# Performance work log

Hardware: AMD Instinct MI355X
Metric: run time of the kernel (lower is better)

## Reference

```python
import jax, jax.numpy as jnp
import numpy as np
from jax import lax

BN_EPS = 1e-5


def ternarize(w):
    """Per-output-channel ternary quantization (Li & Liu TWN style).
    delta_i = 0.7 * mean(|w_i|); alpha_i = mean of |w| over entries with |w| > delta_i;
    output = alpha_i * (+1 where w > delta_i, -1 where w < -delta_i, else 0).
    """
    aw = jnp.abs(w)
    axes = tuple(range(1, w.ndim))
    delta = 0.7 * jnp.mean(aw, axis=axes)            # [O]
    d = delta.reshape((-1,) + (1,) * (w.ndim - 1))   # broadcastable
    mask = aw > d
    alpha = jnp.sum(aw * mask, axis=axes) / jnp.sum(mask, axis=axes)
    tern = jnp.where(w > d, 1.0, 0.0) - jnp.where(w < -d, 1.0, 0.0)
    return tern * alpha.reshape(d.shape)


def batchnorm2d(x, gamma, beta):
    # training-mode batchnorm: batch statistics over (N, H, W), biased variance
    mean = jnp.mean(x, axis=(0, 2, 3), keepdims=True)
    var = jnp.mean((x - mean) ** 2, axis=(0, 2, 3), keepdims=True)
    xhat = (x - mean) * lax.rsqrt(var + BN_EPS)
    return xhat * gamma[None, :, None, None] + beta[None, :, None, None]


def conv2d(x, w, b):
    out = lax.conv_general_dilated(x, w, window_strides=(1, 1), padding='VALID',
                                   dimension_numbers=('NCHW', 'OIHW', 'NCHW'))
    return out + b[None, :, None, None]


def maxpool2(x):
    return lax.reduce_window(x, -jnp.inf, lax.max, (1, 1, 2, 2), (1, 1, 2, 2), 'VALID')


def setup_inputs() -> dict:
    key = jax.random.key(0)
    ks = jax.random.split(key, 10)
    B = 4096
    return {
        'x': jax.random.normal(ks[0], (B, 1, 28, 28), jnp.float32),
        'w_conv1': jax.random.normal(ks[1], (32, 1, 5, 5), jnp.float32) * 0.2,
        'b_conv1': jax.random.normal(ks[2], (32,), jnp.float32) * 0.1,
        'gamma1': jnp.ones((32,), jnp.float32),
        'beta1': jnp.zeros((32,), jnp.float32),
        'w_conv2': jax.random.normal(ks[3], (64, 32, 5, 5), jnp.float32) * 0.05,
        'b_conv2': jax.random.normal(ks[4], (64,), jnp.float32) * 0.1,
        'gamma2': jnp.ones((64,), jnp.float32),
        'beta2': jnp.zeros((64,), jnp.float32),
        'w_fc1': jax.random.normal(ks[5], (512, 1024), jnp.float32) * 0.03,
        'b_fc1': jax.random.normal(ks[6], (512,), jnp.float32) * 0.1,
        'w_fc2': jax.random.normal(ks[7], (10, 512), jnp.float32) * 0.05,
        'b_fc2': jax.random.normal(ks[8], (10,), jnp.float32) * 0.1,
    }


def reference(x, w_conv1, b_conv1, gamma1, beta1, w_conv2, b_conv2, gamma2, beta2,
              w_fc1, b_fc1, w_fc2, b_fc2):
    h = conv2d(x, ternarize(w_conv1), b_conv1)          # [B,32,24,24]
    h = jax.nn.relu(maxpool2(batchnorm2d(h, gamma1, beta1)))  # [B,32,12,12]
    h = conv2d(h, ternarize(w_conv2), b_conv2)          # [B,64,8,8]
    h = jax.nn.relu(maxpool2(batchnorm2d(h, gamma2, beta2)))  # [B,64,4,4]
    h = h.reshape(-1, 1024)
    h = jax.nn.relu(h @ ternarize(w_fc1).T + b_fc1)     # [B,512]
    return h @ ternarize(w_fc2).T + b_fc2               # [B,10]
```

## Files before the change

### kernel.cpp

```cpp
#include <hip/hip_runtime.h>

#define TID ((int)threadIdx.x)
typedef unsigned short ushort_t;
typedef short short8 __attribute__((ext_vector_type(8)));
typedef float f32x4 __attribute__((ext_vector_type(4)));

__device__ __forceinline__ float bf2f(ushort_t u) {
    return __uint_as_float(((unsigned int)u) << 16);
}
__device__ __forceinline__ ushort_t f2bf(float f) {
    unsigned int x = __float_as_uint(f);
    return (ushort_t)((x + 0x7FFFu + ((x >> 16) & 1u)) >> 16);
}
__device__ __forceinline__ float ld1(const void* p, int i, bool f32) {
    return f32 ? ((const float*)p)[i] : bf2f(((const ushort_t*)p)[i]);
}
__device__ __forceinline__ bool probe_f32(const void* g1) {
    return ((const ushort_t*)g1)[0] == 0x0000u;
}

__global__ __launch_bounds__(256) void tern_all_kernel(
    const void* __restrict__ w1, const void* __restrict__ w2,
    const void* __restrict__ wf1, const void* __restrict__ wf2,
    float* __restrict__ o1, float* __restrict__ o2,
    float* __restrict__ of1, float* __restrict__ of2,
    float* __restrict__ stats_z, const void* __restrict__ g1probe)
{
    const bool f32 = probe_f32(g1probe);
    const int blk = blockIdx.x;
    if (blk < 48) stats_z[blk * 256 + TID] = 0.f;

    const void* w; float* out; int K, sk, so, o;
    if (blk < 32)       { w = w1;  out = o1;  K = 25;   sk = 1;  so = 25;   o = blk; }
    else if (blk < 96)  { w = w2;  out = o2;  K = 800;  sk = 64; so = 1;    o = blk - 32; }
    else if (blk < 608) { w = wf1; out = of1; K = 1024; sk = 1;  so = 1024; o = blk - 96; }
    else                { w = wf2; out = of2; K = 512;  sk = 1;  so = 512;  o = blk - 608; }

    const size_t base = (size_t)o * K;
    __shared__ float red[256];
    __shared__ float red2[256];

    float s = 0.f;
    for (int k = TID; k < K; k += 256) s += fabsf(ld1(w, base + k, f32));
    red[TID] = s; __syncthreads();
    for (int st = 128; st > 0; st >>= 1) {
        if (TID < st) red[TID] += red[TID + st];
        __syncthreads();
    }
    const float delta = 0.7f * red[0] / (float)K;
    __syncthreads();

    float ms = 0.f, cnt = 0.f;
    for (int k = TID; k < K; k += 256) {
        float aw = fabsf(ld1(w, base + k, f32));
        if (aw > delta) { ms += aw; cnt += 1.f; }
    }
    red[TID] = ms; red2[TID] = cnt; __syncthreads();
    for (int st = 128; st > 0; st >>= 1) {
        if (TID < st) { red[TID] += red[TID + st]; red2[TID] += red2[TID + st]; }
        __syncthreads();
    }
    const float denom = red2[0];
    const float alpha = (denom > 0.f) ? (red[0] / denom) : 0.f;

    for (int k = TID; k < K; k += 256) {
        float v = ld1(w, base + k, f32);
        float t = (v > delta) ? alpha : ((v < -delta) ? -alpha : 0.f);
        out[(size_t)k * sk + (size_t)o * so] = t;
    }
}

__global__ __launch_bounds__(256) void pack_all_kernel(
    const float* __restrict__ w1t, const float* __restrict__ w2t,
    const float* __restrict__ wf1t, const float* __restrict__ wf2t,
    short8* __restrict__ wpack1, short8* __restrict__ wpack2,
    short8* __restrict__ wf1pack, short8* __restrict__ wf2pack)
{
    const int blk = blockIdx.x;
    if (blk == 0) {
        if (TID < 128) {
            const int nt = TID >> 6, lane = TID & 63;
            const int n = nt * 16 + (lane & 15);
            const int qd = lane >> 4;
            short8 frag;
#pragma unroll
            for (int j = 0; j < 8; ++j) {
                int k = qd * 8 + j, ky = k / 6, kx = k - ky * 6;
                frag[j] = (k < 30 && kx < 5)
                          ? (short)f2bf(w1t[n * 25 + ky * 5 + kx]) : (short)0;
            }
            wpack1[nt * 64 + lane] = frag;
        }
    } else if (blk < 26) {
        const int pos = blk - 1;
        const int nt = TID >> 6, lane = TID & 63;
        const int oc = nt * 16 + (lane & 15);
        short8 frag;
#pragma unroll
        for (int j = 0; j < 8; ++j) {
            int ic = ((lane >> 4) << 3) + j;
            frag[j] = (short)f2bf(w2t[(ic * 25 + pos) * 64 + oc]);
        }
        wpack2[(pos * 4 + nt) * 64 + lane] = frag;
    } else if (blk < 282) {
        const int g = (blk - 26) * 256 + TID;
        const int lane = g & 63;
        const int ntg = (g >> 6) & 31;
        const int kk = g >> 11;
        const int n = ntg * 16 + (lane & 15);
        const int k0 = kk * 32 + ((lane >> 4) << 3);
        short8 frag;
#pragma unroll
        for (int j = 0; j < 8; ++j)
            frag[j] = (short)f2bf(wf1t[(size_t)n * 1024 + k0 + j]);
        wf1pack[g] = frag;
    } else {
        const int lane = TID & 63;
        const int n = lane & 15, qd = lane >> 4;
        for (int kk = TID >> 6; kk < 16; kk += 4) {
            short8 frag;
#pragma unroll
            for (int j = 0; j < 8; ++j)
                frag[j] = (n < 10)
                          ? (short)f2bf(wf2t[n * 512 + kk * 32 + qd * 8 + j])
                          : (short)0;
            wf2pack[kk * 64 + lane] = frag;
        }
    }
}

__device__ __forceinline__ void conv1_koff(int qd, int* koff) {
#pragma unroll
    for (int j = 0; j < 8; ++j) {
        int k = qd * 8 + j, ky = k / 6, kx = k - ky * 6;
        koff[j] = (k < 30 && kx < 5) ? (ky * 28 + kx) : -1;
    }
}

__global__ __launch_bounds__(256) void conv1_stats_kernel(
    const void* __restrict__ x, const short8* __restrict__ wpack1,
    const void* __restrict__ gamma1, float* __restrict__ stats,
    ushort_t* __restrict__ pooled1)
{
    const bool f32 = probe_f32(gamma1);
    __shared__ ushort_t xs[2][784];
    __shared__ float reds[4][64];
    const int b0 = blockIdx.x * 2;
    for (int c = TID; c < 392; c += 256) {
        const int img = (c >= 196) ? 1 : 0;
        const int cc = c - img * 196;
        if (f32) {
            float4 v4 = ((const float4*)x)[(size_t)(b0 + img) * 196 + cc];
            ushort4 u;
            u.x = f2bf(v4.x); u.y = f2bf(v4.y); u.z = f2bf(v4.z); u.w = f2bf(v4.w);
            *(ushort4*)&xs[img][cc * 4] = u;
        } else {
            *(ushort4*)&xs[img][cc * 4] =
                ((const ushort4*)x)[(size_t)(b0 + img) * 196 + cc];
        }
    }
    __syncthreads();

    const int lane = TID & 63, wv = TID >> 6;
    const int img = wv >> 1, wvi = wv & 1;
    const int qd = lane >> 4, ln15 = lane & 15;
    int koff[8];
    conv1_koff(qd, koff);
    const short8 bw0 = wpack1[lane];
    const short8 bw1 = wpack1[64 + lane];
    const bool pos0 = ld1(gamma1, ln15, f32) >= 0.f;
    const bool pos1 = ld1(gamma1, 16 + ln15, f32) >= 0.f;

    float s0 = 0.f, q0 = 0.f, s1 = 0.f, q1 = 0.f;
    const int cellA0 = (ln15 >> 2);
    const int m3 = ln15 & 3;
    const size_t pb = (size_t)(b0 + img) * 144;
    const ushort_t* xsi = xs[img];
    for (int t = wvi * 18; t < wvi * 18 + 18; ++t) {
        const int cellA = t * 4 + cellA0;
        const int pbase = ((cellA / 12) * 2 + (m3 >> 1)) * 28
                        + (cellA % 12) * 2 + (m3 & 1);
        short8 a;
#pragma unroll
        for (int j = 0; j < 8; ++j)
            a[j] = (koff[j] >= 0) ? (short)xsi[pbase + koff[j]] : (short)0;
        f32x4 c0 = {0.f, 0.f, 0.f, 0.f}, c1 = {0.f, 0.f, 0.f, 0.f};
        c0 = __builtin_amdgcn_mfma_f32_16x16x32_bf16(a, bw0, c0, 0, 0, 0);
        c1 = __builtin_amdgcn_mfma_f32_16x16x32_bf16(a, bw1, c1, 0, 0, 0);
#pragma unroll
        for (int r = 0; r < 4; ++r) {
            s0 += c0[r]; q0 += c0[r] * c0[r];
            s1 += c1[r]; q1 += c1[r] * c1[r];
        }
        float mx0 = fmaxf(fmaxf(c0[0], c0[1]), fmaxf(c0[2], c0[3]));
        float mn0 = fminf(fminf(c0[0], c0[1]), fminf(c0[2], c0[3]));
        float mx1 = fmaxf(fmaxf(c1[0], c1[1]), fmaxf(c1[2], c1[3]));
        float mn1 = fminf(fminf(c1[0], c1[1]), fminf(c1[2], c1[3]));
        const int cell = t * 4 + qd;
        pooled1[(pb + cell) * 32 + ln15]      = f2bf(pos0 ? mx0 : mn0);
        pooled1[(pb + cell) * 32 + 16 + ln15] = f2bf(pos1 ? mx1 : mn1);
    }
    s0 += __shfl_xor(s0, 16); q0 += __shfl_xor(q0, 16);
    s1 += __shfl_xor(s1, 16); q1 += __shfl_xor(q1, 16);
    s0 += __shfl_xor(s0, 32); q0 += __shfl_xor(q0, 32);
    s1 += __shfl_xor(s1, 32); q1 += __shfl_xor(q1, 32);
    if (lane < 16) {
        reds[wv][ln15]      = s0;
        reds[wv][32 + ln15] = q0;
        reds[wv][16 + ln15] = s1;
        reds[wv][48 + ln15] = q1;
    }
    __syncthreads();
    if (TID < 64) {
        float v = reds[0][TID] + reds[1][TID] + reds[2][TID] + reds[3][TID];
        atomicAdd(&stats[(blockIdx.x & 63) * 64 + TID], v);
    }
}

__global__ void bnfin_kernel(const float* __restrict__ stats, int C, int slots,
                             float invN,
                             const void* __restrict__ gamma,
                             const void* __restrict__ beta,
                             const void* __restrict__ bias,
                             float* __restrict__ sc, float* __restrict__ sh,
                             const void* __restrict__ g1probe)
{
    const bool f32 = probe_f32(g1probe);
    const int c = TID;
    if (c < C) {
        float s = 0.f, q = 0.f;
        for (int sl = 0; sl < slots; ++sl) {
            s += stats[sl * 2 * C + c];
            q += stats[sl * 2 * C + C + c];
        }
        float mraw = s * invN;
        float var  = q * invN - mraw * mraw;
        float mean = mraw + (bias ? ld1(bias, c, f32) : 0.f);
        float rstd = rsqrtf(fmaxf(var, 0.f) + 1e-5f);
        float g = ld1(gamma, c, f32) * rstd;
        sc[c] = g;
        sh[c] = ld1(beta, c, f32) - mean * g;
    }
}

__global__ __launch_bounds__(256) void conv12_kernel(
    const ushort_t* __restrict__ pooled1,
    const void* __restrict__ b1, const float* __restrict__ sc1,
    const float* __restrict__ sh1, const short8* __restrict__ wpack2,
    const void* __restrict__ b2, const void* __restrict__ gamma2,
    ushort_t* __restrict__ pooled2, float* __restrict__ stats2,
    const void* __restrict__ g1probe)
{
    const bool f32 = probe_f32(g1probe);
    __shared__ ushort_t p1b[144 * 40];
    __shared__ float r2[4][64];
    __shared__ float as1[32], hs1[32];
    const int b = blockIdx.x;
    if (TID < 32) {
        float a = sc1[TID];
        as1[TID] = a;
        hs1[TID] = fmaf(ld1(b1, TID, f32), a, sh1[TID]);
    }
    __syncthreads();

    {
        const uint* pm = (const uint*)(pooled1 + (size_t)b * 4608);
        const int ch2 = (TID * 2) & 31;
        const float aA = as1[ch2],     hA = hs1[ch2];
        const float aB = as1[ch2 + 1], hB = hs1[ch2 + 1];
#pragma unroll
        for (int i = 0; i < 9; ++i) {
            const int idx = i * 256 + TID;
            const uint u = pm[idx];
            const int cell = idx >> 4;
            float v0 = bf2f((ushort_t)(u & 0xFFFFu));
            float v1 = bf2f((ushort_t)(u >> 16));
            uint o0 = f2bf(fmaxf(fmaf(aA, v0, hA), 0.f));
            uint o1 = f2bf(fmaxf(fmaf(aB, v1, hB), 0.f));
            *(uint*)&p1b[cell * 40 + ch2] = o0 | (o1 << 16);
        }
    }
    __syncthreads();

    const int lane = TID & 63, wv = TID >> 6;
    const int qd = lane >> 4, ln15 = lane & 15;
    const int mh = wv >> 1, nh = wv & 1;
    const int px0 = (mh * 2 + 0) * 16 + ln15;
    const int px1 = (mh * 2 + 1) * 16 + ln15;
    const int base0 = (px0 >> 3) * 12 + (px0 & 7);
    const int base1 = (px1 >> 3) * 12 + (px1 & 7);

    f32x4 acc[2][2] = {};
#pragma unroll
    for (int pos = 0; pos < 25; ++pos) {
        const int koff2 = (pos / 5) * 12 + (pos % 5);
        short8 a0 = *(const short8*)&p1b[(base0 + koff2) * 40 + qd * 8];
        short8 a1 = *(const short8*)&p1b[(base1 + koff2) * 40 + qd * 8];
        short8 bb0 = wpack2[(pos * 4 + nh * 2 + 0) * 64 + lane];
        short8 bb1 = wpack2[(pos * 4 + nh * 2 + 1) * 64 + lane];
        acc[0][0] = __builtin_amdgcn_mfma_f32_16x16x32_bf16(a0, bb0, acc[0][0], 0, 0, 0);
        acc[0][1] = __builtin_amdgcn_mfma_f32_16x16x32_bf16(a0, bb1, acc[0][1], 0, 0, 0);
        acc[1][0] = __builtin_amdgcn_mfma_f32_16x16x32_bf16(a1, bb0, acc[1][0], 0, 0, 0);
        acc[1][1] = __builtin_amdgcn_mfma_f32_16x16x32_bf16(a1, bb1, acc[1][1], 0, 0, 0);
    }

    const size_t p2base = (size_t)b * 1024;
#pragma unroll
    for (int jn = 0; jn < 2; ++jn) {
        const int oc = (nh * 2 + jn) * 16 + ln15;
        const float bias = ld1(b2, oc, f32);
        const bool gpos = ld1(gamma2, oc, f32) >= 0.f;
        float s0 = 0.f, q0 = 0.f;
#pragma unroll
        for (int i = 0; i < 2; ++i) {
            float v0 = acc[i][jn][0] + bias;
            float v1 = acc[i][jn][1] + bias;
            float v2 = acc[i][jn][2] + bias;
            float v3 = acc[i][jn][3] + bias;
            s0 += v0 + v1 + v2 + v3;
            q0 += v0*v0 + v1*v1 + v2*v2 + v3*v3;
            float mx01 = fmaxf(v0, v1), mn01 = fminf(v0, v1);
            float mx23 = fmaxf(v2, v3), mn23 = fminf(v2, v3);
            mx01 = fmaxf(mx01, __shfl_xor(mx01, 32));
            mn01 = fminf(mn01, __shfl_xor(mn01, 32));
            mx23 = fmaxf(mx23, __shfl_xor(mx23, 32));
            mn23 = fminf(mn23, __shfl_xor(mn23, 32));
            if (qd < 2) {
                ushort2 st;
                st.x = f2bf(gpos ? mx01 : mn01);
                st.y = f2bf(gpos ? mx23 : mn23);
                const int ti = mh * 2 + i;
                *(ushort2*)&pooled2[p2base + (size_t)oc * 16 + ti * 4 + 2 * qd] = st;
            }
        }
        s0 += __shfl_down(s0, 32); q0 += __shfl_down(q0, 32);
        s0 += __shfl_down(s0, 16); q0 += __shfl_down(q0, 16);
        if (lane < 16) {
            r2[wv][jn * 32 + lane]      = s0;
            r2[wv][jn * 32 + 16 + lane] = q0;
        }
    }
    __syncthreads();
    if (TID < 128) {
        const int idx = TID & 63, nh2 = TID >> 6;
        float v = r2[nh2][idx] + r2[nh2 + 2][idx];
        const int jn = idx >> 5, isq = (idx >> 4) & 1, chx = idx & 15;
        const int oc = nh2 * 32 + jn * 16 + chx;
        atomicAdd(&stats2[(blockIdx.x & 63) * 128 + isq * 64 + oc], v);
    }
}

__global__ __launch_bounds__(256) void fc1_kernel(
    const ushort_t* __restrict__ pooled2, const short8* __restrict__ wf1pack,
    const float* __restrict__ sc2, const float* __restrict__ sh2,
    const void* __restrict__ bias, ushort_t* __restrict__ out,
    const void* __restrict__ g1probe)
{
    const bool f32 = probe_f32(g1probe);
    __shared__ ushort_t As[64 * 136];
    __shared__ float a2s[64], h2s[64];
    const int m0 = blockIdx.y * 64;
    const int n0x4 = blockIdx.x * 4;
    const int lane = TID & 63;
    const int wv   = TID >> 6;
    const int mh = wv >> 1, nh = wv & 1;
    const int qd = lane >> 4, ln15 = lane & 15;
    if (TID < 64) { a2s[TID] = sc2[TID]; h2s[TID] = sh2[TID]; }

    f32x4 acc[2][2] = {};
    for (int stage = 0; stage < 8; ++stage) {
        __syncthreads();
#pragma unroll
        for (int i = 0; i < 4; ++i) {
            const int idx = i * 256 + TID;
            const int row = idx >> 4, ch = idx & 15;
            const int k = stage * 128 + ch * 8;
            const int oc = k >> 4;
            const float a2 = a2s[oc], h2 = h2s[oc];
            uint4 u = *(const uint4*)&pooled2[(size_t)(m0 + row) * 1024 + k];
            uint4 o;
            uint* up = &u.x; uint* op = &o.x;
#pragma unroll
            for (int q = 0; q < 4; ++q) {
                float lo = bf2f((ushort_t)(up[q] & 0xFFFFu));
                float hi = bf2f((ushort_t)(up[q] >> 16));
                uint olo = f2bf(fmaxf(fmaf(a2, lo, h2), 0.f));
                uint ohi = f2bf(fmaxf(fmaf(a2, hi, h2), 0.f));
                op[q] = olo | (ohi << 16);
            }
            *(uint4*)&As[row * 136 + ch * 8] = o;
        }
        __syncthreads();
#pragma unroll
        for (int ks = 0; ks < 4; ++ks) {
            const int kk = stage * 4 + ks;
            const int col = ks * 32 + qd * 8;
            short8 a0 = *(const short8*)&As[(mh * 32 + ln15) * 136 + col];
            short8 a1 = *(const short8*)&As[(mh * 32 + 16 + ln15) * 136 + col];
            short8 bb0 = wf1pack[(kk * 32 + n0x4 + nh * 2 + 0) * 64 + lane];
            short8 bb1 = wf1pack[(kk * 32 + n0x4 + nh * 2 + 1) * 64 + lane];
            acc[0][0] = __builtin_amdgcn_mfma_f32_16x16x32_bf16(a0, bb0, acc[0][0], 0, 0, 0);
            acc[0][1] = __builtin_amdgcn_mfma_f32_16x16x32_bf16(a0, bb1, acc[0][1], 0, 0, 0);
            acc[1][0] = __builtin_amdgcn_mfma_f32_16x16x32_bf16(a1, bb0, acc[1][0], 0, 0, 0);
            acc[1][1] = __builtin_amdgcn_mfma_f32_16x16x32_bf16(a1, bb1, acc[1][1], 0, 0, 0);
        }
    }

#pragma unroll
    for (int jn = 0; jn < 2; ++jn) {
        const int n = n0x4 * 16 + (nh * 2 + jn) * 16 + ln15;
        const float bv = ld1(bias, n, f32);
#pragma unroll
        for (int i = 0; i < 2; ++i) {
            const int mb = m0 + (mh * 2 + i) * 16 + qd * 4;
#pragma unroll
            for (int r = 0; r < 4; ++r) {
                float v = fmaxf(acc[i][jn][r] + bv, 0.f);
                out[(size_t)(mb + r) * 512 + n] = f2bf(v);
            }
        }
    }
}

__global__ __launch_bounds__(256) void fc2_kernel(
    const ushort_t* __restrict__ h, const short8* __restrict__ wf2pack,
    const void* __restrict__ bias, void* __restrict__ out,
    const void* __restrict__ g1probe)
{
    const bool f32 = probe_f32(g1probe);
    const int lane = TID & 63, wv = TID >> 6;
    const int qd = lane >> 4, ln15 = lane & 15;
    const int m0 = (blockIdx.x * 4 + wv) * 16;

    f32x4 acc = {0.f, 0.f, 0.f, 0.f};
#pragma unroll
    for (int kk = 0; kk < 16; ++kk) {
        short8 a = *(const short8*)&h[(size_t)(m0 + ln15) * 512 + kk * 32 + qd * 8];
        acc = __builtin_amdgcn_mfma_f32_16x16x32_bf16(a, wf2pack[kk * 64 + lane],
                                                      acc, 0, 0, 0);
    }
    if (ln15 < 10) {
        const float bv = ld1(bias, ln15, f32);
#pragma unroll
        for (int r = 0; r < 4; ++r) {
            const size_t oi = (size_t)(m0 + qd * 4 + r) * 10 + ln15;
            float v = acc[r] + bv;
            if (f32) ((float*)out)[oi] = v;
            else ((ushort_t*)out)[oi] = f2bf(v);
        }
    }
}

extern "C" void kernel_launch(void* const* d_in, const int* in_sizes, int n_in,
                              void* d_out, int out_size, void* d_ws, size_t ws_size,
                              hipStream_t stream)
{
    const void* x       = d_in[0];
    const void* w_conv1 = d_in[1];
    const void* b_conv1 = d_in[2];
    const void* gamma1  = d_in[3];
    const void* beta1   = d_in[4];
    const void* w_conv2 = d_in[5];
    const void* b_conv2 = d_in[6];
    const void* gamma2  = d_in[7];
    const void* beta2   = d_in[8];
    const void* w_fc1   = d_in[9];
    const void* b_fc1   = d_in[10];
    const void* w_fc2   = d_in[11];
    const void* b_fc2   = d_in[12];

    char* wsb = (char*)d_ws;
    size_t off = 0;
    auto alloc = [&](size_t bytes) -> void* {
        void* p = wsb + off;
        off += (bytes + 255) & ~(size_t)255;
        return p;
    };

    float*  stats   = (float*)alloc(49152);
    float*  stats2  = stats + 4096;
    float*  sc1     = (float*)alloc(128);
    float*  sh1     = (float*)alloc(128);
    float*  sc2     = (float*)alloc(256);
    float*  sh2     = (float*)alloc(256);
    float*  w1t     = (float*)alloc(32 * 25 * 4);
    float*  w2t     = (float*)alloc(800 * 64 * 4);
    float*  wf1t    = (float*)alloc((size_t)512 * 1024 * 4);
    float*  wf2t    = (float*)alloc(10 * 512 * 4);
    short8* wpack1  = (short8*)alloc(2 * 64 * 16);
    short8* wpack2  = (short8*)alloc(25 * 4 * 64 * 16);
    short8* wf1pack = (short8*)alloc((size_t)32 * 32 * 64 * 16);
    short8* wf2pack = (short8*)alloc(16 * 64 * 16);
    ushort_t* pooled1 = (ushort_t*)alloc((size_t)4096 * 144 * 32 * 2);
    ushort_t* pooled2 = (ushort_t*)alloc((size_t)4096 * 64 * 16 * 2);
    ushort_t* fc1o    = (ushort_t*)alloc((size_t)4096 * 512 * 2);

    tern_all_kernel<<<618, 256, 0, stream>>>(w_conv1, w_conv2, w_fc1, w_fc2,
                                             w1t, w2t, wf1t, wf2t, stats, gamma1);
    pack_all_kernel<<<283, 256, 0, stream>>>(w1t, w2t, wf1t, wf2t,
                                             wpack1, wpack2, wf1pack, wf2pack);

    conv1_stats_kernel<<<2048, 256, 0, stream>>>(x, wpack1, gamma1, stats, pooled1);
    bnfin_kernel<<<1, 64, 0, stream>>>(stats, 32, 64, 1.f / 2359296.f,
                                       gamma1, beta1, b_conv1, sc1, sh1, gamma1);

    conv12_kernel<<<4096, 256, 0, stream>>>(pooled1, b_conv1, sc1, sh1,
                                            wpack2, b_conv2, gamma2,
                                            pooled2, stats2, gamma1);
    bnfin_kernel<<<1, 64, 0, stream>>>(stats2, 64, 64, 1.f / 262144.f,
                                       gamma2, beta2, nullptr, sc2, sh2, gamma1);

    fc1_kernel<<<dim3(8, 64), 256, 0, stream>>>(pooled2, wf1pack, sc2, sh2,
                                                b_fc1, fc1o, gamma1);
    fc2_kernel<<<64, 256, 0, stream>>>(fc1o, wf2pack, b_fc2, d_out, gamma1);
}
```

Measured before the change: 220.4 us.

## Fuse ternarize with MFMA packing and fold BN finalize into consumers

The ternarize kernel now writes bf16 values directly into the packed MFMA fragment layouts, which removes the separate pack kernel and the fp32 transposed intermediate buffers. The two single-block BN finalize kernels are dropped. Each conv12 and fc1 block now reduces the per-slot statistics itself and computes scale and shift in shared memory. This cuts three launches and their serialization gaps, but every block redoes the small stats reduction, and the packed writes become scattered 2-byte stores.

New measurement: 192.0 us. -12.9%, faster.

```diff
diff --git a/kernel.cpp b/kernel.cpp
--- a/kernel.cpp
+++ b/kernel.cpp
@@ -19,22 +19,22 @@
     return ((const ushort_t*)g1)[0] == 0x0000u;
 }
 
-__global__ __launch_bounds__(256) void tern_all_kernel(
+__global__ __launch_bounds__(256) void tern_pack_kernel(
     const void* __restrict__ w1, const void* __restrict__ w2,
     const void* __restrict__ wf1, const void* __restrict__ wf2,
-    float* __restrict__ o1, float* __restrict__ o2,
-    float* __restrict__ of1, float* __restrict__ of2,
+    ushort_t* __restrict__ wpack1, ushort_t* __restrict__ wpack2,
+    ushort_t* __restrict__ wf1pack, ushort_t* __restrict__ wf2pack,
     float* __restrict__ stats_z, const void* __restrict__ g1probe)
 {
     const bool f32 = probe_f32(g1probe);
     const int blk = blockIdx.x;
     if (blk < 48) stats_z[blk * 256 + TID] = 0.f;
 
-    const void* w; float* out; int K, sk, so, o;
-    if (blk < 32)       { w = w1;  out = o1;  K = 25;   sk = 1;  so = 25;   o = blk; }
-    else if (blk < 96)  { w = w2;  out = o2;  K = 800;  sk = 64; so = 1;    o = blk - 32; }
-    else if (blk < 608) { w = wf1; out = of1; K = 1024; sk = 1;  so = 1024; o = blk - 96; }
-    else                { w = wf2; out = of2; K = 512;  sk = 1;  so = 512;  o = blk - 608; }
+    const void* w; int K, o, seg;
+    if (blk < 32)       { w = w1;  K = 25;   o = blk;       seg = 0; }
+    else if (blk < 96)  { w = w2;  K = 800;  o = blk - 32;  seg = 1; }
+    else if (blk < 608) { w = wf1; K = 1024; o = blk - 96;  seg = 2; }
+    else                { w = wf2; K = 512;  o = blk - 608; seg = 3; }
 
     const size_t base = (size_t)o * K;
     __shared__ float red[256];
@@ -65,67 +65,25 @@
 
     for (int k = TID; k < K; k += 256) {
         float v = ld1(w, base + k, f32);
-        float t = (v > delta) ? alpha : ((v < -delta) ? -alpha : 0.f);
-        out[(size_t)k * sk + (size_t)o * so] = t;
-    }
-}
-
-__global__ __launch_bounds__(256) void pack_all_kernel(
-    const float* __restrict__ w1t, const float* __restrict__ w2t,
-    const float* __restrict__ wf1t, const float* __restrict__ wf2t,
-    short8* __restrict__ wpack1, short8* __restrict__ wpack2,
-    short8* __restrict__ wf1pack, short8* __restrict__ wf2pack)
-{
-    const int blk = blockIdx.x;
-    if (blk == 0) {
-        if (TID < 128) {
-            const int nt = TID >> 6, lane = TID & 63;
-            const int n = nt * 16 + (lane & 15);
-            const int qd = lane >> 4;
-            short8 frag;
-#pragma unroll
-            for (int j = 0; j < 8; ++j) {
-                int k = qd * 8 + j, ky = k / 6, kx = k - ky * 6;
-                frag[j] = (k < 30 && kx < 5)
-                          ? (short)f2bf(w1t[n * 25 + ky * 5 + kx]) : (short)0;
-            }
-            wpack1[nt * 64 + lane] = frag;
-        }
-    } else if (blk < 26) {
-        const int pos = blk - 1;
-        const int nt = TID >> 6, lane = TID & 63;
-        const int oc = nt * 16 + (lane & 15);
-        short8 frag;
-#pragma unroll
-        for (int j = 0; j < 8; ++j) {
-            int ic = ((lane >> 4) << 3) + j;
-            frag[j] = (short)f2bf(w2t[(ic * 25 + pos) * 64 + oc]);
-        }
-        wpack2[(pos * 4 + nt) * 64 + lane] = frag;
-    } else if (blk < 282) {
-        const int g = (blk - 26) * 256 + TID;
-        const int lane = g & 63;
-        const int ntg = (g >> 6) & 31;
-        const int kk = g >> 11;
-        const int n = ntg * 16 + (lane & 15);
-        const int k0 = kk * 32 + ((lane >> 4) << 3);
-        short8 frag;
-#pragma unroll
-        for (int j = 0; j < 8; ++j)
-            frag[j] = (short)f2bf(wf1t[(size_t)n * 1024 + k0 + j]);
-        wf1pack[g] = frag;
-    } else {
-        const int lane = TID & 63;
-        const int n = lane & 15, qd = lane >> 4;
-        for (int kk = TID >> 6; kk < 16; kk += 4) {
-            short8 frag;
-#pragma unroll
-            for (int j = 0; j < 8; ++j)
-                frag[j] = (n < 10)
-                          ? (short)f2bf(wf2t[n * 512 + kk * 32 + qd * 8 + j])
-                          : (short)0;
-            wf2pack[kk * 64 + lane] = frag;
-        }
+        ushort_t tb = f2bf((v > delta) ? alpha : ((v < -delta) ? -alpha : 0.f));
+        if (seg == 0) {
+            const int kp = (k / 5) * 6 + (k % 5);
+            wpack1[((size_t)(o >> 4) * 64 + (kp >> 3) * 16 + (o & 15)) * 8 + (kp & 7)] = tb;
+        } else if (seg == 1) {
+            const int pos = k % 25, ic = k / 25;
+            wpack2[((size_t)(pos * 4 + (o >> 4)) * 64 + (ic >> 3) * 16 + (o & 15)) * 8
+                   + (ic & 7)] = tb;
+        } else if (seg == 2) {
+            wf1pack[((size_t)((k >> 5) * 32 + (o >> 4)) * 64 + ((k >> 3) & 3) * 16
+                     + (o & 15)) * 8 + (k & 7)] = tb;
+        } else {
+            wf2pack[((size_t)(k >> 5) * 64 + ((k >> 3) & 3) * 16 + o) * 8 + (k & 7)] = tb;
+        }
+    }
+    if (seg == 0 && TID < 7) {
+        const int kps[7] = {5, 11, 17, 23, 29, 30, 31};
+        const int kp = kps[TID];
+        wpack1[((size_t)(o >> 4) * 64 + (kp >> 3) * 16 + (o & 15)) * 8 + (kp & 7)] = 0;
     }
 }
 
@@ -138,11 +96,12 @@
 }
 
 __global__ __launch_bounds__(256) void conv1_stats_kernel(
-    const void* __restrict__ x, const short8* __restrict__ wpack1,
+    const void* __restrict__ x, const ushort_t* __restrict__ wpack1u,
     const void* __restrict__ gamma1, float* __restrict__ stats,
     ushort_t* __restrict__ pooled1)
 {
     const bool f32 = probe_f32(gamma1);
+    const short8* wpack1 = (const short8*)wpack1u;
     __shared__ ushort_t xs[2][784];
     __shared__ float reds[4][64];
     const int b0 = blockIdx.x * 2;
@@ -217,49 +176,39 @@
     }
 }
 
-__global__ void bnfin_kernel(const float* __restrict__ stats, int C, int slots,
-                             float invN,
-                             const void* __restrict__ gamma,
-                             const void* __restrict__ beta,
-                             const void* __restrict__ bias,
-                             float* __restrict__ sc, float* __restrict__ sh,
-                             const void* __restrict__ g1probe)
-{
-    const bool f32 = probe_f32(g1probe);
-    const int c = TID;
-    if (c < C) {
-        float s = 0.f, q = 0.f;
-        for (int sl = 0; sl < slots; ++sl) {
-            s += stats[sl * 2 * C + c];
-            q += stats[sl * 2 * C + C + c];
-        }
+__global__ __launch_bounds__(256) void conv12_kernel(
+    const ushort_t* __restrict__ pooled1, const float* __restrict__ stats,
+    const void* __restrict__ gamma1, const void* __restrict__ beta1,
+    const ushort_t* __restrict__ wpack2u,
+    const void* __restrict__ b2, const void* __restrict__ gamma2,
+    ushort_t* __restrict__ pooled2, float* __restrict__ stats2)
+{
+    const bool f32 = probe_f32(gamma1);
+    const short8* wpack2 = (const short8*)wpack2u;
+    __shared__ ushort_t p1b[144 * 40];
+    __shared__ float r2[4][64];
+    __shared__ float bn4[4][64];
+    __shared__ float as1[32], hs1[32];
+    const int b = blockIdx.x;
+
+    {
+        const int c = TID & 63, g = TID >> 6;
+        float v = 0.f;
+        for (int sl = g; sl < 64; sl += 4) v += stats[sl * 64 + c];
+        bn4[g][c] = v;
+    }
+    __syncthreads();
+    if (TID < 32) {
+        float s = bn4[0][TID] + bn4[1][TID] + bn4[2][TID] + bn4[3][TID];
+        float q = bn4[0][32 + TID] + bn4[1][32 + TID]
+                + bn4[2][32 + TID] + bn4[3][32 + TID];
+        const float invN = 1.f / 2359296.f;
         float mraw = s * invN;
         float var  = q * invN - mraw * mraw;
-        float mean = mraw + (bias ? ld1(bias, c, f32) : 0.f);
         float rstd = rsqrtf(fmaxf(var, 0.f) + 1e-5f);
-        float g = ld1(gamma, c, f32) * rstd;
-        sc[c] = g;
-        sh[c] = ld1(beta, c, f32) - mean * g;
-    }
-}
-
-__global__ __launch_bounds__(256) void conv12_kernel(
-    const ushort_t* __restrict__ pooled1,
-    const void* __restrict__ b1, const float* __restrict__ sc1,
-    const float* __restrict__ sh1, const short8* __restrict__ wpack2,
-    const void* __restrict__ b2, const void* __restrict__ gamma2,
-    ushort_t* __restrict__ pooled2, float* __restrict__ stats2,
-    const void* __restrict__ g1probe)
-{
-    const bool f32 = probe_f32(g1probe);
-    __shared__ ushort_t p1b[144 * 40];
-    __shared__ float r2[4][64];
-    __shared__ float as1[32], hs1[32];
-    const int b = blockIdx.x;
-    if (TID < 32) {
-        float a = sc1[TID];
-        as1[TID] = a;
-        hs1[TID] = fmaf(ld1(b1, TID, f32), a, sh1[TID]);
+        float g1v = ld1(gamma1, TID, f32) * rstd;
+        as1[TID] = g1v;
+        hs1[TID] = ld1(beta1, TID, f32) - mraw * g1v;
     }
     __syncthreads();
 
@@ -351,13 +300,16 @@
 }
 
 __global__ __launch_bounds__(256) void fc1_kernel(
-    const ushort_t* __restrict__ pooled2, const short8* __restrict__ wf1pack,
-    const float* __restrict__ sc2, const float* __restrict__ sh2,
+    const ushort_t* __restrict__ pooled2, const ushort_t* __restrict__ wf1packu,
+    const float* __restrict__ stats2,
+    const void* __restrict__ gamma2, const void* __restrict__ beta2,
     const void* __restrict__ bias, ushort_t* __restrict__ out,
     const void* __restrict__ g1probe)
 {
     const bool f32 = probe_f32(g1probe);
+    const short8* wf1pack = (const short8*)wf1packu;
     __shared__ ushort_t As[64 * 136];
+    __shared__ float bn2[2][128];
     __shared__ float a2s[64], h2s[64];
     const int m0 = blockIdx.y * 64;
     const int n0x4 = blockIdx.x * 4;
@@ -365,7 +317,25 @@
     const int wv   = TID >> 6;
     const int mh = wv >> 1, nh = wv & 1;
     const int qd = lane >> 4, ln15 = lane & 15;
-    if (TID < 64) { a2s[TID] = sc2[TID]; h2s[TID] = sh2[TID]; }
+
+    {
+        const int c = TID & 127, g = TID >> 7;
+        float v = 0.f;
+        for (int sl = g; sl < 64; sl += 2) v += stats2[sl * 128 + c];
+        bn2[g][c] = v;
+    }
+    __syncthreads();
+    if (TID < 64) {
+        float s = bn2[0][TID] + bn2[1][TID];
+        float q = bn2[0][64 + TID] + bn2[1][64 + TID];
+        const float invN = 1.f / 262144.f;
+        float mean = s * invN;
+        float var  = q * invN - mean * mean;
+        float rstd = rsqrtf(fmaxf(var, 0.f) + 1e-5f);
+        float g2 = ld1(gamma2, TID, f32) * rstd;
+        a2s[TID] = g2;
+        h2s[TID] = ld1(beta2, TID, f32) - mean * g2;
+    }
 
     f32x4 acc[2][2] = {};
     for (int stage = 0; stage < 8; ++stage) {
@@ -423,11 +393,12 @@
 }
 
 __global__ __launch_bounds__(256) void fc2_kernel(
-    const ushort_t* __restrict__ h, const short8* __restrict__ wf2pack,
+    const ushort_t* __restrict__ h, const ushort_t* __restrict__ wf2packu,
     const void* __restrict__ bias, void* __restrict__ out,
     const void* __restrict__ g1probe)
 {
     const bool f32 = probe_f32(g1probe);
+    const short8* wf2pack = (const short8*)wf2packu;
     const int lane = TID & 63, wv = TID >> 6;
     const int qd = lane >> 4, ln15 = lane & 15;
     const int m0 = (blockIdx.x * 4 + wv) * 16;
@@ -468,6 +439,7 @@
     const void* b_fc1   = d_in[10];
     const void* w_fc2   = d_in[11];
     const void* b_fc2   = d_in[12];
+    (void)b_conv1;
 
     char* wsb = (char*)d_ws;
     size_t off = 0;
@@ -477,40 +449,27 @@
         return p;
     };
 
-    float*  stats   = (float*)alloc(49152);
-    float*  stats2  = stats + 4096;
-    float*  sc1     = (float*)alloc(128);
-    float*  sh1     = (float*)alloc(128);
-    float*  sc2     = (float*)alloc(256);
-    float*  sh2     = (float*)alloc(256);
-    float*  w1t     = (float*)alloc(32 * 25 * 4);
-    float*  w2t     = (float*)alloc(800 * 64 * 4);
-    float*  wf1t    = (float*)alloc((size_t)512 * 1024 * 4);
-    float*  wf2t    = (float*)alloc(10 * 512 * 4);
-    short8* wpack1  = (short8*)alloc(2 * 64 * 16);
-    short8* wpack2  = (short8*)alloc(25 * 4 * 64 * 16);
-    short8* wf1pack = (short8*)alloc((size_t)32 * 32 * 64 * 16);
-    short8* wf2pack = (short8*)alloc(16 * 64 * 16);
+    float*    stats   = (float*)alloc(49152);
+    float*    stats2  = stats + 4096;
+    ushort_t* wpack1  = (ushort_t*)alloc(2 * 64 * 16);
+    ushort_t* wpack2  = (ushort_t*)alloc(25 * 4 * 64 * 16);
+    ushort_t* wf1pack = (ushort_t*)alloc((size_t)32 * 32 * 64 * 16);
+    ushort_t* wf2pack = (ushort_t*)alloc(16 * 64 * 16);
     ushort_t* pooled1 = (ushort_t*)alloc((size_t)4096 * 144 * 32 * 2);
     ushort_t* pooled2 = (ushort_t*)alloc((size_t)4096 * 64 * 16 * 2);
     ushort_t* fc1o    = (ushort_t*)alloc((size_t)4096 * 512 * 2);
 
-    tern_all_kernel<<<618, 256, 0, stream>>>(w_conv1, w_conv2, w_fc1, w_fc2,
-                                             w1t, w2t, wf1t, wf2t, stats, gamma1);
-    pack_all_kernel<<<283, 256, 0, stream>>>(w1t, w2t, wf1t, wf2t,
-                                             wpack1, wpack2, wf1pack, wf2pack);
+    tern_pack_kernel<<<618, 256, 0, stream>>>(w_conv1, w_conv2, w_fc1, w_fc2,
+                                              wpack1, wpack2, wf1pack, wf2pack,
+                                              stats, gamma1);
 
     conv1_stats_kernel<<<2048, 256, 0, stream>>>(x, wpack1, gamma1, stats, pooled1);
-    bnfin_kernel<<<1, 64, 0, stream>>>(stats, 32, 64, 1.f / 2359296.f,
-                                       gamma1, beta1, b_conv1, sc1, sh1, gamma1);
-
-    conv12_kernel<<<4096, 256, 0, stream>>>(pooled1, b_conv1, sc1, sh1,
+
+    conv12_kernel<<<4096, 256, 0, stream>>>(pooled1, stats, gamma1, beta1,
                                             wpack2, b_conv2, gamma2,
-                                            pooled2, stats2, gamma1);
-    bnfin_kernel<<<1, 64, 0, stream>>>(stats2, 64, 64, 1.f / 262144.f,
-                                       gamma2, beta2, nullptr, sc2, sh2, gamma1);
-
-    fc1_kernel<<<dim3(8, 64), 256, 0, stream>>>(pooled2, wf1pack, sc2, sh2,
-                                                b_fc1, fc1o, gamma1);
+                                            pooled2, stats2);
+
+    fc1_kernel<<<dim3(8, 64), 256, 0, stream>>>(pooled2, wf1pack, stats2,
+                                                gamma2, beta2, b_fc1, fc1o, gamma1);
     fc2_kernel<<<64, 256, 0, stream>>>(fc1o, wf2pack, b_fc2, d_out, gamma1);
 }
```
